# Kernel optimization log

Hardware: AMD Instinct MI355X
Metric: run time of the kernel (lower is better)

The kernel has to match this reference:

```python
import jax, jax.numpy as jnp
import numpy as np
from jax import lax

B, S, D, T = 64, 256, 1024, 60
HIST = 20  # last-20 window of attn / decoder-state history


def setup_inputs() -> dict:
    key = jax.random.key(0)
    ks = jax.random.split(key, 8)
    e_outputs = jax.random.normal(ks[0], (B, S, D), jnp.float32)
    queries = jax.random.normal(ks[1], (B, T, D), jnp.float32)
    # attention weights over source frames: rows sum to 1
    attns = jax.nn.softmax(jax.random.normal(ks[2], (B, T, S), jnp.float32), axis=-1)
    g = 0.02
    Wr = jax.random.normal(ks[3], (D, 1), jnp.float32) * g
    br = jnp.zeros((1,), jnp.float32)
    Wa = jax.random.normal(ks[4], (D, 1), jnp.float32) * g
    ba = jnp.zeros((1,), jnp.float32)
    Wq = jax.random.normal(ks[5], (D, D), jnp.float32) / np.sqrt(D)
    Wn = jax.random.normal(ks[6], (2 * D, 1), jnp.float32) * g
    bn = jnp.zeros((1,), jnp.float32)
    return {"e_outputs": e_outputs, "queries": queries, "attns": attns,
            "Wr": Wr, "br": br, "Wa": Wa, "ba": ba, "Wq": Wq, "Wn": Wn, "bn": bn}


def reference(e_outputs, queries, attns, Wr, br, Wa, ba, Wq, Wn, bn):
    Bn, Sn, Dn = e_outputs.shape
    # decay1[i] = (i+1)/20 ; decay2[i] = 1-(i+1)/50, zero-padded past 50 frames
    decay1 = (jnp.arange(HIST, dtype=jnp.float32) + 1.0) / 20.0
    idx = jnp.arange(Sn, dtype=jnp.float32)
    add0 = jnp.where(idx < 50, 1.0 - (idx + 1.0) / 50.0, 0.0)
    add_state0 = add0[None, :, None]                       # [1,S,1]
    mem0 = e_outputs * add_state0                          # [B,S,D]
    abuf0 = jnp.zeros((HIST, Bn, Sn), e_outputs.dtype)
    qbuf0 = jnp.zeros((HIST, Bn, Dn), e_outputs.dtype)

    def step(carry, x):
        mem, add_state, abuf, qbuf, i = carry
        attn_i, q_i = x                                    # [B,S], [B,D]
        # read: selected frame before memory update
        sel = jnp.einsum('bs,bsd->bd', attn_i, mem)
        # roll history buffers (newest at slot HIST-1)
        abuf = jnp.concatenate([abuf[1:], attn_i[None]], axis=0)
        qbuf = jnp.concatenate([qbuf[1:], q_i[None]], axis=0)
        k = jnp.minimum(i + 1, HIST)
        valid = jnp.arange(HIST) >= (HIST - k)
        temp = jax.nn.softmax(jnp.where(valid, decay1, -jnp.inf))
        attn_w = jnp.einsum('t,tbs->bs', temp, abuf)       # decayed attn sum
        query_s = jnp.einsum('t,tbd->bd', temp, qbuf)      # decayed query sum
        remove_prob = jax.nn.sigmoid(q_i @ Wr + br)[:, :, None]   # [B,1,1]
        add_prob = jax.nn.sigmoid(q_i @ Wa + ba)[:, :, None]      # [B,1,1]
        sim = jax.nn.sigmoid(jnp.einsum('bsd,bd->bs', mem, query_s @ Wq))[..., None]
        mem = mem * (1.0 - remove_prob * attn_w[..., None] * sim)
        last_ctx = jnp.einsum('bs,bsd->bd', attn_w, e_outputs)[:, None, :]
        cat = jnp.concatenate([e_outputs, jnp.broadcast_to(last_ctx, e_outputs.shape)], axis=-1)
        nxt = jax.nn.sigmoid(cat @ Wn + bn)                # [B,S,1]
        mem = mem + e_outputs * (1.0 - add_state) * (add_prob * nxt)
        add_state = add_state + (1.0 - add_state) * (add_prob * nxt)
        return (mem, add_state, abuf, qbuf, i + 1), sel

    init = (mem0, jnp.broadcast_to(add_state0, (Bn, Sn, 1)), abuf0, qbuf0, jnp.int32(0))
    xs = (attns.transpose(1, 0, 2), queries.transpose(1, 0, 2))
    _, sels = lax.scan(step, init, xs)
    return sels.transpose(1, 0, 2)                         # [B,T,D]
```

## Files before the change

kernel.cpp:

```cpp
#include <hip/hip_runtime.h>
#include <math.h>


#define Bn 64
#define Sn 256
#define Dn 1024
#define Tn 60
#define HISTn 20
#define LDK 72
#define K05 1.0512710963760241f
#define EINV 0.36787944117144233f
#define LOG2E 1.4426950408889634f

typedef __bf16 bf16x8 __attribute__((ext_vector_type(8)));
typedef float f32x4 __attribute__((ext_vector_type(4)));
typedef unsigned short us8 __attribute__((ext_vector_type(8)));

typedef const __attribute__((address_space(1))) unsigned int* gas_u32p;
typedef __attribute__((address_space(3))) unsigned int* las_u32p;

__device__ __forceinline__ void gl16(const unsigned short* g, unsigned short* l){
  __builtin_amdgcn_global_load_lds((gas_u32p)g, (las_u32p)l, 16, 0, 0);
}

__device__ __forceinline__ unsigned short f2bf(float f){
  unsigned int x; __builtin_memcpy(&x,&f,4);
  unsigned int lsb = (x >> 16) & 1u;
  x += 0x7fffu + lsb;
  return (unsigned short)(x >> 16);
}
__device__ __forceinline__ float sigmoidf_(float x){
  float e = __builtin_amdgcn_exp2f(-x * LOG2E);
  return __builtin_amdgcn_rcpf(1.0f + e);
}

__global__ __launch_bounds__(256) void convAll(
    const float* __restrict__ Q, const float* __restrict__ Wr,
    const float* __restrict__ br, const float* __restrict__ Wa,
    const float* __restrict__ ba, const float* __restrict__ Wq,
    const float* __restrict__ E, const float* __restrict__ Wn,
    float* __restrict__ rp, float* __restrict__ ap,
    unsigned short* __restrict__ Qbf, unsigned short* __restrict__ WT,
    unsigned short* __restrict__ Ebf,
    float* __restrict__ eW1, float* __restrict__ eW2)
{
  int tid = threadIdx.x;
  int bx = blockIdx.x;
  if (bx < Bn*Tn){
    int row = bx;
    float4 x = ((const float4*)(Q + (size_t)row*Dn))[tid];
    float4 a = ((const float4*)Wr)[tid];
    float4 b = ((const float4*)Wa)[tid];
    unsigned short o[4] = {f2bf(x.x), f2bf(x.y), f2bf(x.z), f2bf(x.w)};
    *(uint2*)&Qbf[(size_t)row*Dn + tid*4] = *(uint2*)o;
    float s1 = x.x*a.x + x.y*a.y + x.z*a.z + x.w*a.w;
    float s2 = x.x*b.x + x.y*b.y + x.z*b.z + x.w*b.w;
    for (int off = 32; off; off >>= 1){
      s1 += __shfl_down(s1, off, 64);
      s2 += __shfl_down(s2, off, 64);
    }
    __shared__ float r1[4], r2[4];
    int lane = tid & 63, wv = tid >> 6;
    if (lane == 0){ r1[wv] = s1; r2[wv] = s2; }
    __syncthreads();
    if (tid == 0){
      rp[row] = sigmoidf_(r1[0]+r1[1]+r1[2]+r1[3] + br[0]);
      ap[row] = sigmoidf_(r2[0]+r2[1]+r2[2]+r2[3] + ba[0]);
    }
  } else if (bx < Bn*Tn + 256){
    __shared__ __align__(16) unsigned short Tt[64][LDK];
    int t = bx - Bn*Tn;
    int n0 = (t >> 4)*64, k0 = (t & 15)*64;
    int kl = tid >> 4, nl4 = (tid & 15)*4;
    #pragma unroll
    for (int it = 0; it < 4; it++){
      int k = kl + it*16;
      float4 v = *(const float4*)&Wq[(size_t)(k0+k)*Dn + n0 + nl4];
      Tt[nl4+0][k] = f2bf(v.x); Tt[nl4+1][k] = f2bf(v.y);
      Tt[nl4+2][k] = f2bf(v.z); Tt[nl4+3][k] = f2bf(v.w);
    }
    __syncthreads();
    int nr = tid >> 2, kg = (tid & 3)*16;
    *(us8*)&WT[(size_t)(n0+nr)*Dn + k0+kg]   = *(us8*)&Tt[nr][kg];
    *(us8*)&WT[(size_t)(n0+nr)*Dn + k0+kg+8] = *(us8*)&Tt[nr][kg+8];
  } else {
    int row = (bx - (Bn*Tn + 256))*4 + (tid >> 6);
    int lane = tid & 63;
    const float* er = E + (size_t)row*Dn;
    unsigned short* ebr = Ebf + (size_t)row*Dn;
    float d1 = 0.f, d2 = 0.f;
    #pragma unroll
    for (int c = 0; c < 4; c++){
      int idx = c*64 + lane;
      float4 v = ((const float4*)er)[idx];
      float4 w1 = ((const float4*)Wn)[idx];
      float4 w2 = ((const float4*)(Wn + Dn))[idx];
      unsigned short o[4] = {f2bf(v.x), f2bf(v.y), f2bf(v.z), f2bf(v.w)};
      ((uint2*)ebr)[idx] = *(uint2*)o;
      d1 += v.x*w1.x + v.y*w1.y + v.z*w1.z + v.w*w1.w;
      d2 += v.x*w2.x + v.y*w2.y + v.z*w2.z + v.w*w2.w;
    }
    #pragma unroll
    for (int off = 32; off; off >>= 1){
      d1 += __shfl_down(d1, off, 64);
      d2 += __shfl_down(d2, off, 64);
    }
    if (lane == 0){ eW1[row] = d1; eW2[row] = d2; }
  }
}

__global__ __launch_bounds__(256) void qw_gemm(
    const unsigned short* __restrict__ Qbf,
    const unsigned short* __restrict__ WT,
    unsigned short* __restrict__ QWbf)
{
  int tid = threadIdx.x;
  __shared__ __align__(16) unsigned short As0_[128*64], Bs0_[128*64];
  __shared__ __align__(16) unsigned short As1_[128*64], Bs1_[128*64];
  int bx = (blockIdx.x & 7)*30 + (blockIdx.x >> 3);
  int m0 = (bx >> 3)*128, n0 = (bx & 7)*128;
  int lane = tid & 63, wave = tid >> 6;
  int quad = lane >> 4, l16 = lane & 15;
  int wr = (wave >> 1)*64, wc = (wave & 1)*64;
  f32x4 acc[4][4];
  #pragma unroll
  for (int mi=0;mi<4;mi++)
    #pragma unroll
    for (int ni=0;ni<4;ni++)
      #pragma unroll
      for (int r=0;r<4;r++) acc[mi][ni][r]=0.f;
  int lr = lane >> 3;
  int scol = ((lane & 7) ^ lr)*8;
  const unsigned short* gA = Qbf + (size_t)(m0 + lr)*Dn + scol;
  const unsigned short* gB = WT  + (size_t)(n0 + lr)*Dn + scol;

  #define STAGE128(K, A_, B_) { \
    _Pragma("unroll") \
    for (int i = 0; i < 4; i++){ \
      int c = wave*4 + i; \
      gl16(gA + (size_t)c*8*Dn + (K), &A_[c*512]); \
      gl16(gB + (size_t)c*8*Dn + (K), &B_[c*512]); \
    } }
  #define COMP128(A_, B_) { \
    _Pragma("unroll") \
    for (int ks = 0; ks < 2; ks++){ \
      bf16x8 af[4], bg[4]; \
      _Pragma("unroll") \
      for (int mi=0;mi<4;mi++){ \
        int mrow = wr + mi*16 + l16; \
        af[mi] = *(const bf16x8*)&A_[mrow*64 + ((ks*32 + quad*8) ^ ((mrow&7)*8))]; \
      } \
      _Pragma("unroll") \
      for (int ni=0;ni<4;ni++){ \
        int nrow = wc + ni*16 + l16; \
        bg[ni] = *(const bf16x8*)&B_[nrow*64 + ((ks*32 + quad*8) ^ ((nrow&7)*8))]; \
      } \
      _Pragma("unroll") \
      for (int mi=0;mi<4;mi++) \
        _Pragma("unroll") \
        for (int ni=0;ni<4;ni++) \
          acc[mi][ni] = __builtin_amdgcn_mfma_f32_16x16x32_bf16(af[mi], bg[ni], acc[mi][ni], 0, 0, 0); \
    } }

  STAGE128(0, As0_, Bs0_);
  __syncthreads();
  #pragma unroll 1
  for (int k0 = 0; k0 < Dn; k0 += 128){
    STAGE128(k0+64, As1_, Bs1_);
    COMP128(As0_, Bs0_);
    __syncthreads();
    if (k0+128 < Dn) STAGE128(k0+128, As0_, Bs0_);
    COMP128(As1_, Bs1_);
    __syncthreads();
  }
  #undef STAGE128
  #undef COMP128

  #pragma unroll
  for (int mi=0;mi<4;mi++)
    #pragma unroll
    for (int ni=0;ni<4;ni++)
      #pragma unroll
      for (int r=0;r<4;r++){
        int m = m0 + wr + mi*16 + quad*4 + r;
        int n = n0 + wc + ni*16 + l16;
        QWbf[(size_t)m*Dn + n] = f2bf(acc[mi][ni][r]);
      }
}

__global__ __launch_bounds__(256) void gemm_g(
    const unsigned short* __restrict__ QWbf,
    const unsigned short* __restrict__ Ebf,
    float* __restrict__ G)
{
  __shared__ __align__(16) unsigned short As0_[64][LDK], As1_[64][LDK];
  __shared__ __align__(16) unsigned short Bs0_[32][LDK], Bs1_[32][LDK];
  int b = blockIdx.x, s0 = blockIdx.y*32;
  int tid = threadIdx.x, lane = tid & 63, wave = tid >> 6;
  int quad = lane >> 4, l16 = lane & 15;
  f32x4 acc[2];
  #pragma unroll
  for (int nt=0;nt<2;nt++)
    #pragma unroll
    for (int r=0;r<4;r++) acc[nt][r]=0.f;
  int sr = tid >> 2, sk = (tid & 3)*16;
  int brw = tid >> 3, bk = (tid & 7)*8;
  const unsigned short* aRow = QWbf + ((size_t)(b*Tn + sr))*Dn;
  const unsigned short* bRow = Ebf  + ((size_t)(b*Sn + s0 + brw))*Dn;

  #define LOADR(K, ra0, ra1, rb0) { \
    if (sr < Tn){ ra0 = *(const us8*)&aRow[(K)+sk]; ra1 = *(const us8*)&aRow[(K)+sk+8]; } \
    else { ra0 = (us8)0; ra1 = (us8)0; } \
    rb0 = *(const us8*)&bRow[(K)+bk]; }
  #define STORER(A_, B_, ra0, ra1, rb0) { \
    *(us8*)&A_[sr][sk]   = ra0; *(us8*)&A_[sr][sk+8] = ra1; \
    *(us8*)&B_[brw][bk]  = rb0; }
  #define COMP_G(A_, B_) { \
    _Pragma("unroll") \
    for (int kk = 0; kk < 64; kk += 32){ \
      bf16x8 a = *(const bf16x8*)&A_[wave*16 + l16][kk + quad*8]; \
      _Pragma("unroll") \
      for (int nt=0;nt<2;nt++){ \
        bf16x8 bb = *(const bf16x8*)&B_[nt*16 + l16][kk + quad*8]; \
        acc[nt] = __builtin_amdgcn_mfma_f32_16x16x32_bf16(a, bb, acc[nt], 0, 0, 0); \
      } \
    } }

  us8 pa0, pa1, pb0, qa0, qa1, qb0;
  LOADR(0, pa0, pa1, pb0);
  STORER(As0_, Bs0_, pa0, pa1, pb0);
  #pragma unroll 1
  for (int k0 = 0; k0 < Dn; k0 += 128){
    LOADR(k0+64, qa0, qa1, qb0);
    __syncthreads();
    COMP_G(As0_, Bs0_);
    STORER(As1_, Bs1_, qa0, qa1, qb0);
    if (k0+128 < Dn) LOADR(k0+128, pa0, pa1, pb0);
    __syncthreads();
    COMP_G(As1_, Bs1_);
    if (k0+128 < Dn) STORER(As0_, Bs0_, pa0, pa1, pb0);
  }
  #undef LOADR
  #undef STORER
  #undef COMP_G

  #pragma unroll
  for (int nt=0;nt<2;nt++)
    #pragma unroll
    for (int r=0;r<4;r++){
      int t = wave*16 + quad*4 + r;
      if (t < Tn) G[((size_t)(b*Tn + t))*Sn + s0 + nt*16 + l16] = acc[nt][r];
    }
}

__global__ __launch_bounds__(256) void scan_s(
    const float* __restrict__ G,
    const float* __restrict__ At,
    const float* __restrict__ rp,
    const float* __restrict__ ap,
    const float* __restrict__ eW1,
    const float* __restrict__ eW2,
    const float* __restrict__ bnp,
    unsigned short* __restrict__ Pbf)
{
  __shared__ float Rsh[Tn], lcs[Tn], rps[Tn], aps[Tn], invd[Tn];
  int b = blockIdx.x, tid = threadIdx.x;
  int lane = tid & 63, wave = tid >> 6;

  float a_[Tn], g_[Tn];
  {
    const float* at_c = At + (size_t)b*Tn*Sn + tid;
    const float* g_c  = G  + (size_t)b*Tn*Sn + tid;
    #pragma unroll
    for (int i = 0; i < Tn; i++){
      a_[i] = at_c[(size_t)i*Sn];
      g_[i] = g_c[(size_t)i*Sn];
    }
  }

  {
    float4 e2v = ((const float4*)(eW2 + (size_t)b*Sn))[lane];
    const float* at_b = At + (size_t)b*Tn*Sn;
    #pragma unroll
    for (int w = 0; w < 15; w++){
      int j = wave + w*4;
      float4 a4 = ((const float4*)(at_b + (size_t)j*Sn))[lane];
      float v = a4.x*e2v.x + a4.y*e2v.y + a4.z*e2v.z + a4.w*e2v.w;
      #pragma unroll
      for (int off = 32; off; off >>= 1) v += __shfl_down(v, off, 64);
      if (lane == 0) Rsh[j] = v;
    }
  }
  if (tid < Tn){
    rps[tid] = rp[b*Tn + tid];
    aps[tid] = ap[b*Tn + tid];
  }
  __syncthreads();

  if (tid < Tn){
    int i = tid;
    int j0 = (i - HISTn + 1 > 0) ? i - HISTn + 1 : 0;
    float num = 0.f, den = 0.f, wj = 1.f;
    #pragma unroll 1
    for (int j = 0; j <= i; j++){
      wj *= K05;
      if (j >= j0){ num += wj * Rsh[j]; den += wj; }
    }
    float inv = __builtin_amdgcn_rcpf(den);
    lcs[i] = num * inv;
    invd[i] = inv;
  }
  __syncthreads();

  {
    int s = tid;
    float M = (s < 50) ? (1.0f - (s+1)/50.0f) : 0.0f;
    float A = M;
    float bnv = bnp[0];
    float e1 = eW1[b*Sn + s];
    unsigned short* P_b = Pbf + (size_t)b*Tn*Sn + s;
    float num_a = 0.f, num_q = 0.f, wi = 1.f;
    #pragma unroll
    for (int i = 0; i < Tn; i++){
      wi *= K05;
      num_a += wi * a_[i];
      num_q += wi * g_[i];
      if (i >= HISTn){
        float wo = wi * EINV;
        num_a -= wo * a_[i-HISTn];
        num_q -= wo * g_[i-HISTn];
      }
      float inv = invd[i];
      float aw = num_a * inv;
      float qd = num_q * inv;
      P_b[(size_t)i*Sn] = f2bf(a_[i] * M);
      float sim = sigmoidf_(M * qd);
      float nxt = sigmoidf_(e1 + lcs[i] + bnv);
      M = M * (1.0f - rps[i] * aw * sim);
      float g = (1.0f - A) * aps[i] * nxt;
      M += g; A += g;
    }
  }
}

__global__ __launch_bounds__(256) void gemm_sels(
    const unsigned short* __restrict__ Pbf,
    const unsigned short* __restrict__ Ebf,
    float* __restrict__ out)
{
  __shared__ __align__(16) unsigned short As_[64][LDK], Bs_[64][LDK];
  int b = blockIdx.x, n0 = blockIdx.y*64;
  int tid = threadIdx.x, lane = tid & 63, wave = tid >> 6;
  int quad = lane >> 4, l16 = lane & 15;
  f32x4 acc[4];
  #pragma unroll
  for (int nt=0;nt<4;nt++)
    #pragma unroll
    for (int r=0;r<4;r++) acc[nt][r]=0.f;
  int sr = tid >> 2, sk = (tid & 3)*16;

  #define SLOAD(K) { \
    if (sr < Tn){ \
      const unsigned short* pp = &Pbf[((size_t)(b*Tn + sr))*Sn + (K)+sk]; \
      pa0 = *(const us8*)pp; pa1 = *(const us8*)(pp+8); \
    } else { pa0 = (us8)0; pa1 = (us8)0; } \
    const unsigned short* ep = &Ebf[((size_t)(b*Sn + (K) + sr))*Dn + n0 + sk]; \
    pe0 = *(const us8*)ep; pe1 = *(const us8*)(ep + 8); }
  #define SSTORE() { \
    *(us8*)&As_[sr][sk]   = pa0; *(us8*)&As_[sr][sk+8] = pa1; \
    _Pragma("unroll") \
    for (int j=0;j<8;j++){ \
      Bs_[sk+j][sr]   = pe0[j]; \
      Bs_[sk+8+j][sr] = pe1[j]; } }
  #define COMP_S() { \
    _Pragma("unroll") \
    for (int kk = 0; kk < 64; kk += 32){ \
      bf16x8 a = *(const bf16x8*)&As_[wave*16 + l16][kk + quad*8]; \
      _Pragma("unroll") \
      for (int nt=0;nt<4;nt++){ \
        bf16x8 bb = *(const bf16x8*)&Bs_[nt*16 + l16][kk + quad*8]; \
        acc[nt] = __builtin_amdgcn_mfma_f32_16x16x32_bf16(a, bb, acc[nt], 0, 0, 0); \
      } \
    } }

  us8 pa0, pa1, pe0, pe1;
  SLOAD(0);
  SSTORE();
  #pragma unroll
  for (int k0 = 0; k0 < Sn; k0 += 64){
    __syncthreads();
    if (k0+64 < Sn) SLOAD(k0+64);
    COMP_S();
    __syncthreads();
    if (k0+64 < Sn) SSTORE();
  }
  #undef SLOAD
  #undef SSTORE
  #undef COMP_S

  #pragma unroll
  for (int nt=0;nt<4;nt++)
    #pragma unroll
    for (int r=0;r<4;r++){
      int t = wave*16 + quad*4 + r;
      int d = n0 + nt*16 + l16;
      if (t < Tn) out[((size_t)(b*Tn + t))*Dn + d] = acc[nt][r];
    }
}

extern "C" void kernel_launch(void* const* d_in, const int* in_sizes, int n_in,
                              void* d_out, int out_size, void* d_ws, size_t ws_size,
                              hipStream_t stream)
{
  const float* E  = (const float*)d_in[0];
  const float* Q  = (const float*)d_in[1];
  const float* At = (const float*)d_in[2];
  const float* Wr = (const float*)d_in[3];
  const float* br = (const float*)d_in[4];
  const float* Wa = (const float*)d_in[5];
  const float* ba = (const float*)d_in[6];
  const float* Wq = (const float*)d_in[7];
  const float* Wn = (const float*)d_in[8];
  const float* bnp= (const float*)d_in[9];

  char* ws = (char*)d_ws;
  float* rp  = (float*)ws; ws += (size_t)Bn*Tn*4;
  float* ap  = (float*)ws; ws += (size_t)Bn*Tn*4;
  float* eW1 = (float*)ws; ws += (size_t)Bn*Sn*4;
  float* eW2 = (float*)ws; ws += (size_t)Bn*Sn*4;
  unsigned short* Qbf  = (unsigned short*)ws; ws += (size_t)Bn*Tn*Dn*2;
  unsigned short* WT   = (unsigned short*)ws; ws += (size_t)Dn*Dn*2;
  unsigned short* QWbf = (unsigned short*)ws; ws += (size_t)Bn*Tn*Dn*2;
  unsigned short* Ebf  = (unsigned short*)ws; ws += (size_t)Bn*Sn*Dn*2;
  float* G = (float*)ws; ws += (size_t)Bn*Tn*Sn*4;
  unsigned short* Pbf = (unsigned short*)ws; ws += (size_t)Bn*Tn*Sn*2;

  convAll<<<Bn*Tn + 256 + Bn*Sn/4, 256, 0, stream>>>(
      Q, Wr, br, Wa, ba, Wq, E, Wn, rp, ap, Qbf, WT, Ebf, eW1, eW2);
  qw_gemm<<<240, 256, 0, stream>>>(Qbf, WT, QWbf);
  gemm_g<<<dim3(Bn, Sn/32), 256, 0, stream>>>(QWbf, Ebf, G);
  scan_s<<<Bn, 256, 0, stream>>>(G, At, rp, ap, eW1, eW2, bnp, Pbf);
  gemm_sels<<<dim3(Bn, Dn/64), 256, 0, stream>>>(Pbf, Ebf, (float*)d_out);
}
```

Before: 186.6 us.

## Fuse scan into gemm_g via last-block counter and halve qw_gemm M tile

The scan_s kernel is folded into gemm_g: each of the 8 s-tile blocks for a batch atomically increments a per-batch counter after writing G, and the last block to arrive runs the sequential scan for that batch. This removes one kernel launch and its launch gap. The counters are reset inside qw_gemm. Separately, qw_gemm now uses 64-row M tiles with 480 blocks instead of 240, giving more parallelism across CUs. The fused path puts the scan's register-heavy arrays into gemm_g, which may raise its register use and lower occupancy, and it relies on threadfence/atomic ordering for correctness.

```diff
diff --git a/kernel.cpp b/kernel.cpp
--- a/kernel.cpp
+++ b/kernel.cpp
@@ -112,19 +112,21 @@
 __global__ __launch_bounds__(256) void qw_gemm(
     const unsigned short* __restrict__ Qbf,
     const unsigned short* __restrict__ WT,
-    unsigned short* __restrict__ QWbf)
+    unsigned short* __restrict__ QWbf,
+    unsigned int* __restrict__ cnt)
 {
   int tid = threadIdx.x;
-  __shared__ __align__(16) unsigned short As0_[128*64], Bs0_[128*64];
-  __shared__ __align__(16) unsigned short As1_[128*64], Bs1_[128*64];
-  int bx = (blockIdx.x & 7)*30 + (blockIdx.x >> 3);
-  int m0 = (bx >> 3)*128, n0 = (bx & 7)*128;
+  if (tid == 0 && blockIdx.x < Bn) cnt[blockIdx.x] = 0;
+  __shared__ __align__(16) unsigned short As0_[64*64],  Bs0_[128*64];
+  __shared__ __align__(16) unsigned short As1_[64*64],  Bs1_[128*64];
+  int bx = (blockIdx.x & 7)*60 + (blockIdx.x >> 3);
+  int m0 = (bx >> 3)*64, n0 = (bx & 7)*128;
   int lane = tid & 63, wave = tid >> 6;
   int quad = lane >> 4, l16 = lane & 15;
-  int wr = (wave >> 1)*64, wc = (wave & 1)*64;
-  f32x4 acc[4][4];
-  #pragma unroll
-  for (int mi=0;mi<4;mi++)
+  int wr = (wave >> 1)*32, wc = (wave & 1)*64;
+  f32x4 acc[2][4];
+  #pragma unroll
+  for (int mi=0;mi<2;mi++)
     #pragma unroll
     for (int ni=0;ni<4;ni++)
       #pragma unroll
@@ -134,19 +136,23 @@
   const unsigned short* gA = Qbf + (size_t)(m0 + lr)*Dn + scol;
   const unsigned short* gB = WT  + (size_t)(n0 + lr)*Dn + scol;
 
-  #define STAGE128(K, A_, B_) { \
+  #define STAGE64(K, A_, B_) { \
+    _Pragma("unroll") \
+    for (int i = 0; i < 2; i++){ \
+      int c = wave*2 + i; \
+      gl16(gA + (size_t)c*8*Dn + (K), &A_[c*512]); \
+    } \
     _Pragma("unroll") \
     for (int i = 0; i < 4; i++){ \
       int c = wave*4 + i; \
-      gl16(gA + (size_t)c*8*Dn + (K), &A_[c*512]); \
       gl16(gB + (size_t)c*8*Dn + (K), &B_[c*512]); \
     } }
-  #define COMP128(A_, B_) { \
+  #define COMP64(A_, B_) { \
     _Pragma("unroll") \
     for (int ks = 0; ks < 2; ks++){ \
-      bf16x8 af[4], bg[4]; \
+      bf16x8 af[2], bg[4]; \
       _Pragma("unroll") \
-      for (int mi=0;mi<4;mi++){ \
+      for (int mi=0;mi<2;mi++){ \
         int mrow = wr + mi*16 + l16; \
         af[mi] = *(const bf16x8*)&A_[mrow*64 + ((ks*32 + quad*8) ^ ((mrow&7)*8))]; \
       } \
@@ -156,28 +162,28 @@
         bg[ni] = *(const bf16x8*)&B_[nrow*64 + ((ks*32 + quad*8) ^ ((nrow&7)*8))]; \
       } \
       _Pragma("unroll") \
-      for (int mi=0;mi<4;mi++) \
+      for (int mi=0;mi<2;mi++) \
         _Pragma("unroll") \
         for (int ni=0;ni<4;ni++) \
           acc[mi][ni] = __builtin_amdgcn_mfma_f32_16x16x32_bf16(af[mi], bg[ni], acc[mi][ni], 0, 0, 0); \
     } }
 
-  STAGE128(0, As0_, Bs0_);
+  STAGE64(0, As0_, Bs0_);
   __syncthreads();
   #pragma unroll 1
   for (int k0 = 0; k0 < Dn; k0 += 128){
-    STAGE128(k0+64, As1_, Bs1_);
-    COMP128(As0_, Bs0_);
-    __syncthreads();
-    if (k0+128 < Dn) STAGE128(k0+128, As0_, Bs0_);
-    COMP128(As1_, Bs1_);
-    __syncthreads();
-  }
-  #undef STAGE128
-  #undef COMP128
-
-  #pragma unroll
-  for (int mi=0;mi<4;mi++)
+    STAGE64(k0+64, As1_, Bs1_);
+    COMP64(As0_, Bs0_);
+    __syncthreads();
+    if (k0+128 < Dn) STAGE64(k0+128, As0_, Bs0_);
+    COMP64(As1_, Bs1_);
+    __syncthreads();
+  }
+  #undef STAGE64
+  #undef COMP64
+
+  #pragma unroll
+  for (int mi=0;mi<2;mi++)
     #pragma unroll
     for (int ni=0;ni<4;ni++)
       #pragma unroll
@@ -191,7 +197,15 @@
 __global__ __launch_bounds__(256) void gemm_g(
     const unsigned short* __restrict__ QWbf,
     const unsigned short* __restrict__ Ebf,
-    float* __restrict__ G)
+    const float* __restrict__ At,
+    const float* __restrict__ rp,
+    const float* __restrict__ ap,
+    const float* __restrict__ eW1,
+    const float* __restrict__ eW2,
+    const float* __restrict__ bnp,
+    float* __restrict__ G,
+    unsigned short* __restrict__ Pbf,
+    unsigned int* __restrict__ cnt)
 {
   __shared__ __align__(16) unsigned short As0_[64][LDK], As1_[64][LDK];
   __shared__ __align__(16) unsigned short Bs0_[32][LDK], Bs1_[32][LDK];
@@ -251,22 +265,18 @@
       int t = wave*16 + quad*4 + r;
       if (t < Tn) G[((size_t)(b*Tn + t))*Sn + s0 + nt*16 + l16] = acc[nt][r];
     }
-}
-
-__global__ __launch_bounds__(256) void scan_s(
-    const float* __restrict__ G,
-    const float* __restrict__ At,
-    const float* __restrict__ rp,
-    const float* __restrict__ ap,
-    const float* __restrict__ eW1,
-    const float* __restrict__ eW2,
-    const float* __restrict__ bnp,
-    unsigned short* __restrict__ Pbf)
-{
+
+  __threadfence();
+  __shared__ unsigned int lastFlag;
+  if (tid == 0){
+    unsigned int v = atomicAdd(&cnt[b], 1u);
+    lastFlag = (v == 7u);
+  }
+  __syncthreads();
+  if (!lastFlag) return;
+  __threadfence();
+
   __shared__ float Rsh[Tn], lcs[Tn], rps[Tn], aps[Tn], invd[Tn];
-  int b = blockIdx.x, tid = threadIdx.x;
-  int lane = tid & 63, wave = tid >> 6;
-
   float a_[Tn], g_[Tn];
   {
     const float* at_c = At + (size_t)b*Tn*Sn + tid;
@@ -277,7 +287,6 @@
       g_[i] = g_c[(size_t)i*Sn];
     }
   }
-
   {
     float4 e2v = ((const float4*)(eW2 + (size_t)b*Sn))[lane];
     const float* at_b = At + (size_t)b*Tn*Sn;
@@ -296,7 +305,6 @@
     aps[tid] = ap[b*Tn + tid];
   }
   __syncthreads();
-
   if (tid < Tn){
     int i = tid;
     int j0 = (i - HISTn + 1 > 0) ? i - HISTn + 1 : 0;
@@ -311,7 +319,6 @@
     invd[i] = inv;
   }
   __syncthreads();
-
   {
     int s = tid;
     float M = (s < 50) ? (1.0f - (s+1)/50.0f) : 0.0f;
@@ -434,11 +441,12 @@
   unsigned short* Ebf  = (unsigned short*)ws; ws += (size_t)Bn*Sn*Dn*2;
   float* G = (float*)ws; ws += (size_t)Bn*Tn*Sn*4;
   unsigned short* Pbf = (unsigned short*)ws; ws += (size_t)Bn*Tn*Sn*2;
+  unsigned int* cnt = (unsigned int*)ws; ws += (size_t)Bn*4;
 
   convAll<<<Bn*Tn + 256 + Bn*Sn/4, 256, 0, stream>>>(
       Q, Wr, br, Wa, ba, Wq, E, Wn, rp, ap, Qbf, WT, Ebf, eW1, eW2);
-  qw_gemm<<<240, 256, 0, stream>>>(Qbf, WT, QWbf);
-  gemm_g<<<dim3(Bn, Sn/32), 256, 0, stream>>>(QWbf, Ebf, G);
-  scan_s<<<Bn, 256, 0, stream>>>(G, At, rp, ap, eW1, eW2, bnp, Pbf);
+  qw_gemm<<<480, 256, 0, stream>>>(Qbf, WT, QWbf, cnt);
+  gemm_g<<<dim3(Bn, Sn/32), 256, 0, stream>>>(
+      QWbf, Ebf, At, rp, ap, eW1, eW2, bnp, G, Pbf, cnt);
   gemm_sels<<<dim3(Bn, Dn/64), 256, 0, stream>>>(Pbf, Ebf, (float*)d_out);
 }
```

Result: slower. 236.0 us (+26.5%).
